# Optimization experiments

Measured on AMD Instinct MI355X. Metric: run time of the kernel, lower is better.

## Reference

```python
import jax, jax.numpy as jnp
import numpy as np

B, S, VD, MD = 32, 2048, 512, 512
AD = max(VD, MD)


def setup_inputs() -> dict:
    key = jax.random.key(0)
    k1, k2, k3, k4, k5, k6 = jax.random.split(key, 6)
    query = jax.random.normal(k1, (B, VD), dtype=jnp.float32)
    keys = jax.random.normal(k2, (B, S, MD), dtype=jnp.float32)
    mask = jax.random.randint(k3, (B, S), 0, 2).astype(jnp.bool_)
    # torch Linear weight layout: [out, in]
    W1 = jax.random.normal(k4, (AD, VD), dtype=jnp.float32) * (1.0 / np.sqrt(VD))
    W2 = jax.random.normal(k5, (AD, MD), dtype=jnp.float32) * (1.0 / np.sqrt(MD))
    v = jax.random.normal(k6, (AD,), dtype=jnp.float32) * (1.0 / np.sqrt(AD))
    return {"query": query, "keys": keys, "mask": mask, "W1": W1, "W2": W2, "v": v}


def reference(query, keys, mask, W1, W2, v):
    # w1_query: [B, 1, AD]; w2_keys: [B, S, AD]
    w1_query = jnp.einsum('bd,ad->ba', query, W1)[:, None, :]
    w2_keys = jnp.einsum('bsd,ad->bsa', keys, W2)
    combined = jnp.tanh(w1_query + w2_keys)            # [B, S, AD]
    scores = jnp.einsum('bsa,a->bs', combined, v)      # [B, S]
    scores = jnp.where(mask, scores, -jnp.inf)
    attn_weights = jax.nn.softmax(scores, axis=-1)
    return attn_weights
```

## Files before the change

kernel.cpp:

```cpp
#include <hip/hip_runtime.h>
#include <math.h>

#define BB 32
#define SS 2048
#define DD 512
#define AD 512

#define BM 128
#define BN 128
#define BK 64

typedef __bf16 bf16;
typedef __attribute__((ext_vector_type(8))) __bf16 bf16x8;
typedef __attribute__((ext_vector_type(4))) __bf16 bf16x4;
typedef __attribute__((ext_vector_type(4))) float floatx4;

__device__ inline void async16(const void* g, void* l) {
    __builtin_amdgcn_global_load_lds(
        (const __attribute__((address_space(1))) unsigned int*)g,
        (__attribute__((address_space(3))) unsigned int*)l, 16, 0, 0);
}

#define NK8 (BB * SS * DD / 8)
#define NW8 (AD * DD / 8)
#define NCV ((NK8 + NW8) / 256)
__global__ void prep_kernel(const float* __restrict__ keys,
                            const float* __restrict__ W2,
                            bf16* __restrict__ keysb,
                            bf16* __restrict__ W2b,
                            const unsigned char* __restrict__ m8,
                            int* __restrict__ flag,
                            const float* __restrict__ query,
                            const float* __restrict__ W1,
                            float* __restrict__ w1q) {
    const int bid = blockIdx.x;
    if (bid < NCV) {
        int i = threadIdx.x + bid * 256;
        const float* src;
        bf16* dst;
        int j;
        if (i < NK8) { src = keys; dst = keysb; j = i; }
        else         { src = W2;   dst = W2b;   j = i - NK8; }
        const float4* s4 = (const float4*)src + (size_t)j * 2;
        float4 x = s4[0], y = s4[1];
        bf16x8 o;
        o[0] = (bf16)x.x; o[1] = (bf16)x.y; o[2] = (bf16)x.z; o[3] = (bf16)x.w;
        o[4] = (bf16)y.x; o[5] = (bf16)y.y; o[6] = (bf16)y.z; o[7] = (bf16)y.w;
        *(bf16x8*)(dst + (size_t)j * 8) = o;
    } else if (bid < NCV + 64) {
        int t = threadIdx.x + (bid - NCV) * 256;
        int any = 0;
        for (int i = t; i < BB * SS; i += 64 * 256)
            if ((i & 3) && m8[i]) any = 1;
        if (__any(any)) {
            if ((threadIdx.x & 63) == 0) atomicOr(flag, 1);
        }
    } else {
        int id = bid - NCV - 64;
        int b = id >> 7;
        int a = (id & 127) * 4 + (threadIdx.x >> 6);
        int lane = threadIdx.x & 63;
        const float4* q4 = (const float4*)(query + (size_t)b * DD) + lane * 2;
        const float4* w4 = (const float4*)(W1 + (size_t)a * DD) + lane * 2;
        float4 qa = q4[0], qb = q4[1];
        float4 wa = w4[0], wb = w4[1];
        float acc = qa.x * wa.x + qa.y * wa.y + qa.z * wa.z + qa.w * wa.w
                  + qb.x * wb.x + qb.y * wb.y + qb.z * wb.z + qb.w * wb.w;
#pragma unroll
        for (int off = 32; off > 0; off >>= 1) acc += __shfl_down(acc, off);
        if (lane == 0) w1q[(size_t)b * AD + a] = acc;
    }
}

__global__ __launch_bounds__(256, 4)
void gemm_scores_mfma(const bf16* __restrict__ keysb,
                      const bf16* __restrict__ W2b,
                      const float* __restrict__ w1q,
                      const float* __restrict__ v,
                      float* __restrict__ partial) {
    __shared__ bf16 a_lds[BM * BK];
    __shared__ bf16 b_lds[BN * BK];

    const int t    = threadIdx.x;
    const int lane = t & 63;
    const int w    = t >> 6;
    const int ml   = lane & 15;
    const int kg   = lane >> 4;

    const int lin    = blockIdx.x;
    const int x8     = lin & 7;
    const int hi     = lin >> 3;
    const int a_tile = hi & 3;
    const int kt     = x8 + ((hi >> 2) << 3);
    const int b      = kt >> 4;
    const int s0     = (kt & 15) * BM;
    const int a0     = a_tile * BN;

    const int m_off = (w & 1) * 64;
    const int n_off = (w >> 1) * 64;

    const bf16* Ablk = keysb + ((size_t)b * SS + s0) * DD;
    const bf16* Bblk = W2b + (size_t)a0 * DD;

    floatx4 acc[4][4];
#pragma unroll
    for (int mi = 0; mi < 4; ++mi)
#pragma unroll
        for (int ni = 0; ni < 4; ++ni)
            acc[mi][ni] = (floatx4)(0.f);

    const int NCHUNK = DD / BK;
    for (int c = 0; c < NCHUNK; ++c) {
        const int d0 = c * BK;
        __syncthreads();
#pragma unroll
        for (int i = 0; i < 4; ++i) {
            int lin2 = t + 256 * i;
            int r = lin2 >> 3, cc = lin2 & 7, cs = cc ^ (r & 7);
            async16(Ablk + (size_t)r * DD + d0 + cs * 8,
                    &a_lds[(256 * i + w * 64) * 8]);
            async16(Bblk + (size_t)r * DD + d0 + cs * 8,
                    &b_lds[(256 * i + w * 64) * 8]);
        }
        __syncthreads();

#pragma unroll
        for (int ks = 0; ks < 2; ++ks) {
            bf16x8 af[4], bfr[4];
#pragma unroll
            for (int mi = 0; mi < 4; ++mi) {
                int R = m_off + mi * 16 + ml;
                int pos = (ks * 4 + kg) ^ (R & 7);
                af[mi] = *(const bf16x8*)&a_lds[R * BK + pos * 8];
            }
#pragma unroll
            for (int ni = 0; ni < 4; ++ni) {
                int R = n_off + ni * 16 + ml;
                int pos = (ks * 4 + kg) ^ (R & 7);
                bfr[ni] = *(const bf16x8*)&b_lds[R * BK + pos * 8];
            }
#pragma unroll
            for (int mi = 0; mi < 4; ++mi)
#pragma unroll
                for (int ni = 0; ni < 4; ++ni)
                    acc[mi][ni] = __builtin_amdgcn_mfma_f32_16x16x32_bf16(
                        af[mi], bfr[ni], acc[mi][ni], 0, 0, 0);
        }
    }

    float w1qa[4], va[4];
#pragma unroll
    for (int ni = 0; ni < 4; ++ni) {
        int a = a0 + n_off + ni * 16 + ml;
        w1qa[ni] = w1q[(size_t)b * AD + a];
        va[ni]   = v[a];
    }
    const int slot = a_tile * 2 + (w >> 1);
#pragma unroll
    for (int mi = 0; mi < 4; ++mi) {
#pragma unroll
        for (int reg = 0; reg < 4; ++reg) {
            float p = 0.f;
#pragma unroll
            for (int ni = 0; ni < 4; ++ni) {
                float x = acc[mi][ni][reg] + w1qa[ni];
                float th = 1.f - 2.f / (1.f + __expf(2.f * x));
                p = fmaf(th, va[ni], p);
            }
            p += __shfl_xor(p, 1);
            p += __shfl_xor(p, 2);
            p += __shfl_xor(p, 4);
            p += __shfl_xor(p, 8);
            if (ml == 0) {
                int row = m_off + mi * 16 + kg * 4 + reg;
                partial[((size_t)b * SS + s0 + row) * 8 + slot] = p;
            }
        }
    }
}

#define FBK 32
#define FLDK (FBK + 8)
__global__ __launch_bounds__(256, 2)
void gemm_scores_fallback(const float* __restrict__ keys,
                          const float* __restrict__ W2,
                          const float* __restrict__ w1q,
                          const float* __restrict__ v,
                          float* __restrict__ partial) {
    __shared__ bf16 a_lds[BM][FLDK];
    __shared__ bf16 b_lds[BN][FLDK];
    __shared__ float s_red[BM];

    const int t    = threadIdx.x;
    const int lane = t & 63;
    const int w    = t >> 6;
    const int ml   = lane & 15;
    const int kg   = lane >> 4;
    const int b    = blockIdx.z;
    const int s0   = blockIdx.x * BM;
    const int a0   = blockIdx.y * BN;
    const int m_off = (w & 1) * 64;
    const int n_off = (w >> 1) * 64;

    const float* Ablk = keys + ((size_t)b * SS + s0) * DD;
    const float* Bblk = W2 + (size_t)a0 * DD;

    if (t < BM) s_red[t] = 0.f;

    floatx4 acc[4][4];
#pragma unroll
    for (int mi = 0; mi < 4; ++mi)
#pragma unroll
        for (int ni = 0; ni < 4; ++ni)
            acc[mi][ni] = (floatx4)(0.f);

    float4 ga[4], gb[4];
#pragma unroll
    for (int i = 0; i < 4; ++i) {
        int idx = t + 256 * i;
        int r = idx >> 3, c = idx & 7;
        ga[i] = *(const float4*)(Ablk + (size_t)r * DD + c * 4);
        gb[i] = *(const float4*)(Bblk + (size_t)r * DD + c * 4);
    }

    for (int chunk = 0; chunk < DD / FBK; ++chunk) {
        __syncthreads();
#pragma unroll
        for (int i = 0; i < 4; ++i) {
            int idx = t + 256 * i;
            int r = idx >> 3, c = idx & 7;
            bf16x4 pa, pb;
            pa[0] = (bf16)ga[i].x; pa[1] = (bf16)ga[i].y;
            pa[2] = (bf16)ga[i].z; pa[3] = (bf16)ga[i].w;
            pb[0] = (bf16)gb[i].x; pb[1] = (bf16)gb[i].y;
            pb[2] = (bf16)gb[i].z; pb[3] = (bf16)gb[i].w;
            *(bf16x4*)&a_lds[r][c * 4] = pa;
            *(bf16x4*)&b_lds[r][c * 4] = pb;
        }
        __syncthreads();
        if (chunk < DD / FBK - 1) {
            int d0 = (chunk + 1) * FBK;
#pragma unroll
            for (int i = 0; i < 4; ++i) {
                int idx = t + 256 * i;
                int r = idx >> 3, c = idx & 7;
                ga[i] = *(const float4*)(Ablk + (size_t)r * DD + d0 + c * 4);
                gb[i] = *(const float4*)(Bblk + (size_t)r * DD + d0 + c * 4);
            }
        }
        bf16x8 af[4], bfr[4];
#pragma unroll
        for (int mi = 0; mi < 4; ++mi)
            af[mi] = *(const bf16x8*)&a_lds[m_off + mi * 16 + ml][kg * 8];
#pragma unroll
        for (int ni = 0; ni < 4; ++ni)
            bfr[ni] = *(const bf16x8*)&b_lds[n_off + ni * 16 + ml][kg * 8];
#pragma unroll
        for (int mi = 0; mi < 4; ++mi)
#pragma unroll
            for (int ni = 0; ni < 4; ++ni)
                acc[mi][ni] = __builtin_amdgcn_mfma_f32_16x16x32_bf16(
                    af[mi], bfr[ni], acc[mi][ni], 0, 0, 0);
    }

    float w1qa[4], va[4];
#pragma unroll
    for (int ni = 0; ni < 4; ++ni) {
        int a = a0 + n_off + ni * 16 + ml;
        w1qa[ni] = w1q[(size_t)b * AD + a];
        va[ni]   = v[a];
    }
#pragma unroll
    for (int mi = 0; mi < 4; ++mi) {
#pragma unroll
        for (int reg = 0; reg < 4; ++reg) {
            float p = 0.f;
#pragma unroll
            for (int ni = 0; ni < 4; ++ni) {
                float x = acc[mi][ni][reg] + w1qa[ni];
                float th = 1.f - 2.f / (1.f + __expf(2.f * x));
                p = fmaf(th, va[ni], p);
            }
            p += __shfl_xor(p, 1);
            p += __shfl_xor(p, 2);
            p += __shfl_xor(p, 4);
            p += __shfl_xor(p, 8);
            if (ml == 0)
                atomicAdd(&s_red[m_off + mi * 16 + kg * 4 + reg], p);
        }
    }
    __syncthreads();
    if (t < BM)
        partial[(((size_t)b * SS) + s0 + t) * 8 + blockIdx.y * 2] = s_red[t];
}

__global__ void softmax_kernel(const float* __restrict__ partial,
                               const int* __restrict__ mask_i32,
                               const unsigned char* __restrict__ mask_u8,
                               const int* __restrict__ flag,
                               float* __restrict__ out) {
    const int b = blockIdx.x;
    const int t = threadIdx.x;
    __shared__ float rmax[4], rsum[4];
    const int wid = t >> 6, lane = t & 63;

    float sv[8]; int mv[8];
    const int bytes = (*flag != 0);
#pragma unroll
    for (int k = 0; k < 8; ++k) {
        int i = t + 256 * k;
        const float4* p4 = (const float4*)(partial + ((size_t)b * SS + i) * 8);
        float4 pa = p4[0], pb = p4[1];
        sv[k] = ((pa.x + pa.y) + (pa.z + pa.w)) + ((pb.x + pb.y) + (pb.z + pb.w));
        mv[k] = bytes ? (int)mask_u8[(size_t)b * SS + i]
                      : mask_i32[(size_t)b * SS + i];
    }

    float mx = -INFINITY;
#pragma unroll
    for (int k = 0; k < 8; ++k) mx = fmaxf(mx, mv[k] ? sv[k] : -INFINITY);
#pragma unroll
    for (int off = 32; off > 0; off >>= 1) mx = fmaxf(mx, __shfl_xor(mx, off));
    if (lane == 0) rmax[wid] = mx;
    __syncthreads();
    mx = fmaxf(fmaxf(rmax[0], rmax[1]), fmaxf(rmax[2], rmax[3]));

    float ev[8]; float sum = 0.f;
#pragma unroll
    for (int k = 0; k < 8; ++k) {
        ev[k] = mv[k] ? __expf(sv[k] - mx) : 0.f;
        sum += ev[k];
    }
#pragma unroll
    for (int off = 32; off > 0; off >>= 1) sum += __shfl_xor(sum, off);
    if (lane == 0) rsum[wid] = sum;
    __syncthreads();
    sum = (rsum[0] + rsum[1]) + (rsum[2] + rsum[3]);
    float inv = 1.f / sum;
#pragma unroll
    for (int k = 0; k < 8; ++k)
        out[(size_t)b * SS + t + 256 * k] = ev[k] * inv;
}

extern "C" void kernel_launch(void* const* d_in, const int* in_sizes, int n_in,
                              void* d_out, int out_size, void* d_ws, size_t ws_size,
                              hipStream_t stream) {
    const float* query = (const float*)d_in[0];
    const float* keys  = (const float*)d_in[1];
    const void*  mask  = d_in[2];
    const float* W1    = (const float*)d_in[3];
    const float* W2    = (const float*)d_in[4];
    const float* v     = (const float*)d_in[5];
    float* out = (float*)d_out;

    char* wsb = (char*)d_ws;
    int*   flag    = (int*)wsb;
    float* w1q     = (float*)(wsb + 256);
    float* partial = (float*)(wsb + 256 + 65536);
    bf16*  keysb   = (bf16*)(wsb + 256 + 65536 + 2097152);
    bf16*  W2b     = (bf16*)(wsb + 256 + 65536 + 2097152 + (size_t)BB * SS * DD * 2);
    size_t need = 256 + 65536 + 2097152 + (size_t)BB * SS * DD * 2 + (size_t)AD * DD * 2;

    hipMemsetAsync(flag, 0, 4, stream);
    if (ws_size >= need) {
        prep_kernel<<<NCV + 64 + 4096, 256, 0, stream>>>(
            keys, W2, keysb, W2b, (const unsigned char*)mask, flag, query, W1, w1q);
        gemm_scores_mfma<<<(SS / BM) * (AD / BN) * BB, 256, 0, stream>>>(
            keysb, W2b, w1q, v, partial);
    } else {
        hipMemsetAsync(partial, 0, (size_t)BB * SS * 8 * 4, stream);
        prep_kernel<<<64 + 4096, 256, 0, stream>>>(
            keys, W2, keysb, W2b, (const unsigned char*)mask, flag, query, W1, w1q);
        gemm_scores_fallback<<<dim3(SS / BM, AD / BN, BB), 256, 0, stream>>>(
            keys, W2, w1q, v, partial);
    }
    softmax_kernel<<<BB, 256, 0, stream>>>(partial, (const int*)mask,
                                           (const unsigned char*)mask, flag, out);
}
```

Measured before the change: 263.6 us.

## Fuse fp32-to-bf16 key conversion into GEMM LDS load path

Removes the separate pass that converted the full keys tensor to bf16 in a workspace buffer. The GEMM now async-loads fp32 keys straight into LDS with a 16-way XOR swizzle and converts to bf16 while building MFMA fragments. This drops a full read and write of keys plus the re-read of the bf16 copy. In exchange the A tile doubles in LDS size and gathers twice the global bytes per tile, so launch bounds drop to 3 blocks per CU and each fragment load needs extra conversion instructions. The A tile is still re-read from global once per AD tile, now at fp32 width.

```diff
diff --git a/kernel.cpp b/kernel.cpp
--- a/kernel.cpp
+++ b/kernel.cpp
@@ -21,12 +21,9 @@
         (__attribute__((address_space(3))) unsigned int*)l, 16, 0, 0);
 }
 
-#define NK8 (BB * SS * DD / 8)
 #define NW8 (AD * DD / 8)
-#define NCV ((NK8 + NW8) / 256)
-__global__ void prep_kernel(const float* __restrict__ keys,
-                            const float* __restrict__ W2,
-                            bf16* __restrict__ keysb,
+#define NCV (NW8 / 256)
+__global__ void prep_kernel(const float* __restrict__ W2,
                             bf16* __restrict__ W2b,
                             const unsigned char* __restrict__ m8,
                             int* __restrict__ flag,
@@ -35,18 +32,13 @@
                             float* __restrict__ w1q) {
     const int bid = blockIdx.x;
     if (bid < NCV) {
-        int i = threadIdx.x + bid * 256;
-        const float* src;
-        bf16* dst;
-        int j;
-        if (i < NK8) { src = keys; dst = keysb; j = i; }
-        else         { src = W2;   dst = W2b;   j = i - NK8; }
-        const float4* s4 = (const float4*)src + (size_t)j * 2;
+        int j = threadIdx.x + bid * 256;
+        const float4* s4 = (const float4*)W2 + (size_t)j * 2;
         float4 x = s4[0], y = s4[1];
         bf16x8 o;
         o[0] = (bf16)x.x; o[1] = (bf16)x.y; o[2] = (bf16)x.z; o[3] = (bf16)x.w;
         o[4] = (bf16)y.x; o[5] = (bf16)y.y; o[6] = (bf16)y.z; o[7] = (bf16)y.w;
-        *(bf16x8*)(dst + (size_t)j * 8) = o;
+        *(bf16x8*)(W2b + (size_t)j * 8) = o;
     } else if (bid < NCV + 64) {
         int t = threadIdx.x + (bid - NCV) * 256;
         int any = 0;
@@ -72,14 +64,14 @@
     }
 }
 
-__global__ __launch_bounds__(256, 4)
-void gemm_scores_mfma(const bf16* __restrict__ keysb,
+__global__ __launch_bounds__(256, 3)
+void gemm_scores_mfma(const float* __restrict__ keys,
                       const bf16* __restrict__ W2b,
                       const float* __restrict__ w1q,
                       const float* __restrict__ v,
                       float* __restrict__ partial) {
-    __shared__ bf16 a_lds[BM * BK];
-    __shared__ bf16 b_lds[BN * BK];
+    __shared__ float a_lds[BM * BK];
+    __shared__ bf16  b_lds[BN * BK];
 
     const int t    = threadIdx.x;
     const int lane = t & 63;
@@ -99,8 +91,8 @@
     const int m_off = (w & 1) * 64;
     const int n_off = (w >> 1) * 64;
 
-    const bf16* Ablk = keysb + ((size_t)b * SS + s0) * DD;
-    const bf16* Bblk = W2b + (size_t)a0 * DD;
+    const float* Ablk = keys + ((size_t)b * SS + s0) * DD;
+    const bf16*  Bblk = W2b + (size_t)a0 * DD;
 
     floatx4 acc[4][4];
 #pragma unroll
@@ -114,13 +106,18 @@
         const int d0 = c * BK;
         __syncthreads();
 #pragma unroll
+        for (int i = 0; i < 8; ++i) {
+            int g = t + 256 * i;
+            int r = g >> 4, cc = g & 15, cs = cc ^ (r & 15);
+            async16(Ablk + (size_t)r * DD + d0 + cs * 4,
+                    &a_lds[(256 * i + 64 * w) * 4]);
+        }
+#pragma unroll
         for (int i = 0; i < 4; ++i) {
-            int lin2 = t + 256 * i;
-            int r = lin2 >> 3, cc = lin2 & 7, cs = cc ^ (r & 7);
-            async16(Ablk + (size_t)r * DD + d0 + cs * 8,
-                    &a_lds[(256 * i + w * 64) * 8]);
+            int g = t + 256 * i;
+            int r = g >> 3, cc = g & 7, cs = cc ^ (r & 7);
             async16(Bblk + (size_t)r * DD + d0 + cs * 8,
-                    &b_lds[(256 * i + w * 64) * 8]);
+                    &b_lds[(256 * i + 64 * w) * 8]);
         }
         __syncthreads();
 
@@ -129,9 +126,16 @@
             bf16x8 af[4], bfr[4];
 #pragma unroll
             for (int mi = 0; mi < 4; ++mi) {
-                int R = m_off + mi * 16 + ml;
-                int pos = (ks * 4 + kg) ^ (R & 7);
-                af[mi] = *(const bf16x8*)&a_lds[R * BK + pos * 8];
+                int R  = m_off + mi * 16 + ml;
+                int gB = 8 * ks + 2 * kg;
+                float4 lo = *(const float4*)&a_lds[R * BK + ((gB    ) ^ (R & 15)) * 4];
+                float4 hi4 = *(const float4*)&a_lds[R * BK + ((gB + 1) ^ (R & 15)) * 4];
+                bf16x8 f;
+                f[0] = (bf16)lo.x;  f[1] = (bf16)lo.y;
+                f[2] = (bf16)lo.z;  f[3] = (bf16)lo.w;
+                f[4] = (bf16)hi4.x; f[5] = (bf16)hi4.y;
+                f[6] = (bf16)hi4.z; f[7] = (bf16)hi4.w;
+                af[mi] = f;
             }
 #pragma unroll
             for (int ni = 0; ni < 4; ++ni) {
@@ -357,20 +361,19 @@
     int*   flag    = (int*)wsb;
     float* w1q     = (float*)(wsb + 256);
     float* partial = (float*)(wsb + 256 + 65536);
-    bf16*  keysb   = (bf16*)(wsb + 256 + 65536 + 2097152);
-    bf16*  W2b     = (bf16*)(wsb + 256 + 65536 + 2097152 + (size_t)BB * SS * DD * 2);
-    size_t need = 256 + 65536 + 2097152 + (size_t)BB * SS * DD * 2 + (size_t)AD * DD * 2;
+    bf16*  W2b     = (bf16*)(wsb + 256 + 65536 + 2097152);
+    size_t need = 256 + 65536 + 2097152 + (size_t)AD * DD * 2;
 
     hipMemsetAsync(flag, 0, 4, stream);
     if (ws_size >= need) {
         prep_kernel<<<NCV + 64 + 4096, 256, 0, stream>>>(
-            keys, W2, keysb, W2b, (const unsigned char*)mask, flag, query, W1, w1q);
+            W2, W2b, (const unsigned char*)mask, flag, query, W1, w1q);
         gemm_scores_mfma<<<(SS / BM) * (AD / BN) * BB, 256, 0, stream>>>(
-            keysb, W2b, w1q, v, partial);
+            keys, W2b, w1q, v, partial);
     } else {
         hipMemsetAsync(partial, 0, (size_t)BB * SS * 8 * 4, stream);
-        prep_kernel<<<64 + 4096, 256, 0, stream>>>(
-            keys, W2, keysb, W2b, (const unsigned char*)mask, flag, query, W1, w1q);
+        prep_kernel<<<NCV + 64 + 4096, 256, 0, stream>>>(
+            W2, W2b, (const unsigned char*)mask, flag, query, W1, w1q);
         gemm_scores_fallback<<<dim3(SS / BM, AD / BN, BB), 256, 0, stream>>>(
             keys, W2, w1q, v, partial);
     }
```

Result: faster. 245.2 us (-7.0%).
